# Performance work log

Hardware: AMD Instinct MI355X
Metric: run time of the kernel (lower is better)

The kernel has to match this reference:

```python
import jax, jax.numpy as jnp
from jax import lax
import numpy as np

WIN = 11
SIGMA = 1.5
PAD = WIN // 2
C1 = 0.01 ** 2
C2 = 0.03 ** 2


def _gauss1d():
    x = jnp.arange(WIN, dtype=jnp.float32) - (WIN // 2)
    k = jnp.exp(-(x ** 2) / (2.0 * SIGMA ** 2))
    return k / k.sum()


def _blur3d(x, k1d):
    # Separable 3D gaussian blur (mathematically identical to the outer-product
    # 3D kernel used by the torch module, since kernel3d = k1d (x) k1d (x) k1d).
    # x: [B, 1, D, H, W]
    dn = ('NCDHW', 'OIDHW', 'NCDHW')
    x = lax.conv_general_dilated(x, k1d.reshape(1, 1, WIN, 1, 1), (1, 1, 1),
                                 [(PAD, PAD), (0, 0), (0, 0)], dimension_numbers=dn)
    x = lax.conv_general_dilated(x, k1d.reshape(1, 1, 1, WIN, 1), (1, 1, 1),
                                 [(0, 0), (PAD, PAD), (0, 0)], dimension_numbers=dn)
    x = lax.conv_general_dilated(x, k1d.reshape(1, 1, 1, 1, WIN), (1, 1, 1),
                                 [(0, 0), (0, 0), (PAD, PAD)], dimension_numbers=dn)
    return x


def setup_inputs() -> dict:
    key = jax.random.key(0)
    k1, k2 = jax.random.split(key)
    shape = (2, 1, 192, 192, 192)
    img1 = jax.random.uniform(k1, shape, dtype=jnp.float32)
    img2 = jax.random.uniform(k2, shape, dtype=jnp.float32)
    return {"img1": img1, "img2": img2}


def reference(img1, img2):
    k1d = _gauss1d().astype(img1.dtype)
    mu1 = _blur3d(img1, k1d)
    mu2 = _blur3d(img2, k1d)
    mu1_sq = mu1 * mu1
    mu2_sq = mu2 * mu2
    mu1mu2 = mu1 * mu2
    sigma1 = _blur3d(img1 * img1, k1d) - mu1_sq
    sigma2 = _blur3d(img2 * img2, k1d) - mu2_sq
    sigma12 = _blur3d(img1 * img2, k1d) - mu1mu2
    num = (2.0 * mu1mu2 + C1) * (2.0 * sigma12 + C2)
    den = (mu1_sq + mu2_sq + C1) * (sigma1 + sigma2 + C2)
    ssim_map = num / den
    return ssim_map.mean()  # size_average=True
```

## Files before the change

### kernel.cpp

```cpp
#include <hip/hip_runtime.h>

#define NB 2
#define DD 192
#define HH 192
#define WW 192
#define HWSZ (HH * WW)
#define C1F 0.0001f
#define C2F 0.0009f

#define TH 16
#define TW 32
#define CHUNK 32
#define TSTEPS (CHUNK + 10)
#define NCH (DD / CHUNK)
#define NTH (HH / TH)
#define NTW (WW / TW)
#define NBLK (NB * NCH * NTH * NTW)

#define SROWS (TH + 10)
#define SCOLS 42
#define SP2 44
#define TQ 36
#define NSTG (SROWS * SCOLS)
#define NWT (SROWS * (TW / 4))

#define KWLIST { 0.00102838f, 0.00759876f, 0.03600077f, 0.10936071f, 0.21300556f, \
                 0.26601172f, 0.21300556f, 0.10936071f, 0.03600077f, 0.00759876f, 0.00102838f }

__device__ __forceinline__ float ssim_val(float mu1, float mu2, float A, float Bm) {
  const float mu1sq = mu1 * mu1, mu2sq = mu2 * mu2, mu12 = mu1 * mu2;
  const float num = (2.f * mu12 + C1F) * (0.5f * (A - Bm) - 2.f * mu12 + C2F);
  const float den = (mu1sq + mu2sq + C1F) * (0.5f * (A + Bm) - mu1sq - mu2sq + C2F);
  return num * __builtin_amdgcn_rcpf(den);
}

__global__ __launch_bounds__(256) void ssim_fused(
    const float* __restrict__ x, const float* __restrict__ y,
    float* __restrict__ partials) {
  const float KW[11] = KWLIST;

  int bid = blockIdx.x;
  const int tw = bid % NTW; bid /= NTW;
  const int th = bid % NTH; bid /= NTH;
  const int c  = bid % NCH; bid /= NCH;
  const int b  = bid;
  const int h0 = th * TH, w0 = tw * TW, c0 = c * CHUNK;

  __shared__ __align__(16) float2 s2[SROWS][SP2];
  __shared__ float4 t4[SROWS][TQ];

  const int tid = threadIdx.x;
  const int cl  = tid & 31;
  const int rg  = tid >> 5;
  const int r0  = 2 * rg;
  const int clp2 = (cl & ~3) | (((cl & 3) + (cl >> 2)) & 3);

  int  sIdx[5], sOff[5];
  bool sOk[5];
#pragma unroll
  for (int k = 0; k < 5; ++k) {
    const int q = tid + 256 * k;
    const bool act = (q < NSTG);
    const int row = q / SCOLS, col = q % SCOLS;
    const int gh = h0 - 5 + row, gw = w0 - 5 + col;
    sOk[k]  = act && (unsigned)gh < (unsigned)HH && (unsigned)gw < (unsigned)WW;
    sIdx[k] = row * SP2 + col;
    sOff[k] = gh * WW + gw;
  }
  const bool wAct = (tid < NWT);
  const int  wr = tid >> 3;
  const int  wq = tid & 7;
  const int  tBase = wr * TQ + 4 * wq;
  const int  st0 = tBase + ((0 + wq) & 3);
  const int  st1 = tBase + ((1 + wq) & 3);
  const int  st2 = tBase + ((2 + wq) & 3);
  const int  st3 = tBase + ((3 + wq) & 3);

  {
    const float2 z = make_float2(0.f, 0.f);
    for (int q = tid; q < SROWS * SP2; q += 256) (&s2[0][0])[q] = z;
  }
  __syncthreads();

  const float* xb = x + (size_t)b * DD * HWSZ;
  const float* yb = y + (size_t)b * DD * HWSZ;

  float pend0[4][11], pend1[4][11];
#pragma unroll
  for (int f = 0; f < 4; ++f)
#pragma unroll
    for (int i = 0; i < 11; ++i) { pend0[f][i] = 0.f; pend1[f][i] = 0.f; }

  float px[5], py[5];
#pragma unroll
  for (int k = 0; k < 5; ++k) { px[k] = 0.f; py[k] = 0.f; }

  if (c0 >= 5) {
    const float* xs = xb + (size_t)(c0 - 5) * HWSZ;
    const float* ys = yb + (size_t)(c0 - 5) * HWSZ;
#pragma unroll
    for (int k = 0; k < 5; ++k)
      if (sOk[k]) { px[k] = xs[sOff[k]]; py[k] = ys[sOff[k]]; }
  }

  float lsum = 0.f;
  int p = 0;

  for (int t = 0; t < TSTEPS; ++t) {
    const int d = c0 - 5 + t;
    const bool dv = (d >= 0) && (d < DD);

    if (dv) {
#pragma unroll
      for (int k = 0; k < 5; ++k)
        if (sOk[k]) (&s2[0][0])[sIdx[k]] = make_float2(px[k], py[k]);
    }
    {
      const int dn = d + 1;
      if ((t + 1) < TSTEPS && dn >= 0 && dn < DD) {
        const float* xs = xb + (size_t)dn * HWSZ;
        const float* ys = yb + (size_t)dn * HWSZ;
#pragma unroll
        for (int k = 0; k < 5; ++k)
          if (sOk[k]) { px[k] = xs[sOff[k]]; py[k] = ys[sOff[k]]; }
      }
    }

    float4 B0 = make_float4(0.f, 0.f, 0.f, 0.f);
    float4 B1 = B0;

    if (dv) {
      __syncthreads();
      if (wAct) {
        const float4* srow4 = (const float4*)&s2[wr][0];
        float4 a0 = make_float4(0.f, 0.f, 0.f, 0.f), a1 = a0, a2 = a0, a3 = a0;
#pragma unroll
        for (int u2 = 0; u2 < 7; ++u2) {
          const float4 v2 = srow4[2 * wq + u2];
#pragma unroll
          for (int h = 0; h < 2; ++h) {
            const int   u  = 2 * u2 + h;
            const float xx = h ? v2.z : v2.x;
            const float yy = h ? v2.w : v2.y;
            const float sm = xx + yy, df = xx - yy;
            const float s2q = sm * sm, d2q = df * df;
            if (u <= 10)           { const float k = KW[u];     a0.x += k*xx; a0.y += k*yy; a0.z += k*s2q; a0.w += k*d2q; }
            if (u >= 1 && u <= 11) { const float k = KW[u - 1]; a1.x += k*xx; a1.y += k*yy; a1.z += k*s2q; a1.w += k*d2q; }
            if (u >= 2 && u <= 12) { const float k = KW[u - 2]; a2.x += k*xx; a2.y += k*yy; a2.z += k*s2q; a2.w += k*d2q; }
            if (u >= 3)            { const float k = KW[u - 3]; a3.x += k*xx; a3.y += k*yy; a3.z += k*s2q; a3.w += k*d2q; }
          }
        }
        float4* tb = &t4[0][0];
        tb[st0] = a0; tb[st1] = a1; tb[st2] = a2; tb[st3] = a3;
      }
      __syncthreads();

#pragma unroll
      for (int u = 0; u < 12; ++u) {
        const float4 v = t4[r0 + u][clp2];
        if (u <= 10) { const float k = KW[u];     B0.x += k*v.x; B0.y += k*v.y; B0.z += k*v.z; B0.w += k*v.w; }
        if (u >= 1)  { const float k = KW[u - 1]; B1.x += k*v.x; B1.y += k*v.y; B1.z += k*v.z; B1.w += k*v.w; }
      }
    }

#define RING_CASE(P)                                                        \
    case P: {                                                               \
      if (dv) {                                                             \
        _Pragma("unroll")                                                   \
        for (int kk = 0; kk < 11; ++kk) {                                   \
          const int   sl = (P + 1 + kk) % 11;                               \
          const float wg = KW[kk];                                          \
          pend0[0][sl] += wg * B0.x; pend0[1][sl] += wg * B0.y;             \
          pend0[2][sl] += wg * B0.z; pend0[3][sl] += wg * B0.w;             \
          pend1[0][sl] += wg * B1.x; pend1[1][sl] += wg * B1.y;             \
          pend1[2][sl] += wg * B1.z; pend1[3][sl] += wg * B1.w;             \
        }                                                                   \
      }                                                                     \
      const int sc = (P + 1) % 11;                                          \
      if (t >= 10) {                                                        \
        lsum += ssim_val(pend0[0][sc], pend0[1][sc], pend0[2][sc], pend0[3][sc]); \
        lsum += ssim_val(pend1[0][sc], pend1[1][sc], pend1[2][sc], pend1[3][sc]); \
      }                                                                     \
      pend0[0][sc] = 0.f; pend0[1][sc] = 0.f;                               \
      pend0[2][sc] = 0.f; pend0[3][sc] = 0.f;                               \
      pend1[0][sc] = 0.f; pend1[1][sc] = 0.f;                               \
      pend1[2][sc] = 0.f; pend1[3][sc] = 0.f;                               \
    } break;

    switch (p) {
      RING_CASE(0) RING_CASE(1) RING_CASE(2) RING_CASE(3) RING_CASE(4)
      RING_CASE(5) RING_CASE(6) RING_CASE(7) RING_CASE(8) RING_CASE(9)
      RING_CASE(10)
    }
#undef RING_CASE
    p = (p + 1 == 11) ? 0 : p + 1;
  }

  for (int off = 32; off > 0; off >>= 1) lsum += __shfl_down(lsum, off, 64);
  __shared__ float wsum[4];
  if ((tid & 63) == 0) wsum[tid >> 6] = lsum;
  __syncthreads();
  if (tid == 0) partials[blockIdx.x] = wsum[0] + wsum[1] + wsum[2] + wsum[3];
}

__global__ __launch_bounds__(256) void ssim_reduce(
    const float* __restrict__ partials, float* __restrict__ out) {
  __shared__ double sd[256];
  double a = 0.0;
  for (int i = threadIdx.x; i < NBLK; i += 256) a += (double)partials[i];
  sd[threadIdx.x] = a;
  __syncthreads();
  for (int s = 128; s > 0; s >>= 1) {
    if ((int)threadIdx.x < s) sd[threadIdx.x] += sd[threadIdx.x + s];
    __syncthreads();
  }
  if (threadIdx.x == 0) {
    out[0] = (float)(sd[0] / (double)((size_t)NB * DD * HH * WW));
  }
}

extern "C" void kernel_launch(void* const* d_in, const int* in_sizes, int n_in,
                              void* d_out, int out_size, void* d_ws, size_t ws_size,
                              hipStream_t stream) {
  const float* img1 = (const float*)d_in[0];
  const float* img2 = (const float*)d_in[1];
  float* out = (float*)d_out;
  float* partials = (float*)d_ws;

  ssim_fused<<<NBLK, 256, 0, stream>>>(img1, img2, partials);
  ssim_reduce<<<1, 256, 0, stream>>>(partials, out);
}
```

Measured before the change: 171.9 us.

## Double-buffer staging and W-blur shared buffers to pipeline depth slices

Double-buffers the input staging and W-blur shared-memory tiles so that each depth step stages slice e+2, runs the W-blur on slice e+1 and does the H-blur on slice e, all in one phase. This cuts the two barriers per depth step down to one and lets the prefetch run one slice further ahead. It also adds a per-row 2-float skew to the staging layout, apparently to spread LDS bank accesses. The cost is double the shared-memory footprint, which may reduce occupancy, plus a more complex prologue.

```diff
diff --git a/kernel.cpp b/kernel.cpp
--- a/kernel.cpp
+++ b/kernel.cpp
@@ -46,8 +46,8 @@
   const int b  = bid;
   const int h0 = th * TH, w0 = tw * TW, c0 = c * CHUNK;
 
-  __shared__ __align__(16) float2 s2[SROWS][SP2];
-  __shared__ float4 t4[SROWS][TQ];
+  __shared__ __align__(16) float2 s2[2][SROWS][SP2];
+  __shared__ float4 t4[2][SROWS][TQ];
 
   const int tid = threadIdx.x;
   const int cl  = tid & 31;
@@ -64,7 +64,7 @@
     const int row = q / SCOLS, col = q % SCOLS;
     const int gh = h0 - 5 + row, gw = w0 - 5 + col;
     sOk[k]  = act && (unsigned)gh < (unsigned)HH && (unsigned)gw < (unsigned)WW;
-    sIdx[k] = row * SP2 + col;
+    sIdx[k] = row * SP2 + 2 * (row & 1) + col;
     sOff[k] = gh * WW + gw;
   }
   const bool wAct = (tid < NWT);
@@ -78,86 +78,93 @@
 
   {
     const float2 z = make_float2(0.f, 0.f);
-    for (int q = tid; q < SROWS * SP2; q += 256) (&s2[0][0])[q] = z;
-  }
-  __syncthreads();
+    float2* sb = &s2[0][0][0];
+    for (int q = tid; q < 2 * SROWS * SP2; q += 256) sb[q] = z;
+  }
 
   const float* xb = x + (size_t)b * DD * HWSZ;
   const float* yb = y + (size_t)b * DD * HWSZ;
 
-  float pend0[4][11], pend1[4][11];
-#pragma unroll
-  for (int f = 0; f < 4; ++f)
-#pragma unroll
-    for (int i = 0; i < 11; ++i) { pend0[f][i] = 0.f; pend1[f][i] = 0.f; }
-
   float px[5], py[5];
 #pragma unroll
   for (int k = 0; k < 5; ++k) { px[k] = 0.f; py[k] = 0.f; }
 
-  if (c0 >= 5) {
-    const float* xs = xb + (size_t)(c0 - 5) * HWSZ;
-    const float* ys = yb + (size_t)(c0 - 5) * HWSZ;
+  auto do_prefetch = [&](int g) {
+    const float* xs = xb + (size_t)g * HWSZ;
+    const float* ys = yb + (size_t)g * HWSZ;
 #pragma unroll
     for (int k = 0; k < 5; ++k)
       if (sOk[k]) { px[k] = xs[sOff[k]]; py[k] = ys[sOff[k]]; }
-  }
+  };
+  auto do_stage = [&](float2* s2buf) {
+#pragma unroll
+    for (int k = 0; k < 5; ++k)
+      if (sOk[k]) s2buf[sIdx[k]] = make_float2(px[k], py[k]);
+  };
+  auto do_wblur = [&](const float2* s2buf, float4* t4buf) {
+    if (wAct) {
+      const float4* srow4 = (const float4*)(s2buf + wr * SP2 + 2 * (wr & 1));
+      float4 a0 = make_float4(0.f, 0.f, 0.f, 0.f), a1 = a0, a2 = a0, a3 = a0;
+#pragma unroll
+      for (int u2 = 0; u2 < 7; ++u2) {
+        const float4 v2 = srow4[2 * wq + u2];
+#pragma unroll
+        for (int h = 0; h < 2; ++h) {
+          const int   u  = 2 * u2 + h;
+          const float xx = h ? v2.z : v2.x;
+          const float yy = h ? v2.w : v2.y;
+          const float sm = xx + yy, df = xx - yy;
+          const float sq = sm * sm, dq = df * df;
+          if (u <= 10)           { const float k = KW[u];     a0.x += k*xx; a0.y += k*yy; a0.z += k*sq; a0.w += k*dq; }
+          if (u >= 1 && u <= 11) { const float k = KW[u - 1]; a1.x += k*xx; a1.y += k*yy; a1.z += k*sq; a1.w += k*dq; }
+          if (u >= 2 && u <= 12) { const float k = KW[u - 2]; a2.x += k*xx; a2.y += k*yy; a2.z += k*sq; a2.w += k*dq; }
+          if (u >= 3)            { const float k = KW[u - 3]; a3.x += k*xx; a3.y += k*yy; a3.z += k*sq; a3.w += k*dq; }
+        }
+      }
+      t4buf[st0] = a0; t4buf[st1] = a1; t4buf[st2] = a2; t4buf[st3] = a3;
+    }
+  };
+
+  float pend0[4][11], pend1[4][11];
+#pragma unroll
+  for (int f = 0; f < 4; ++f)
+#pragma unroll
+    for (int i = 0; i < 11; ++i) { pend0[f][i] = 0.f; pend1[f][i] = 0.f; }
 
   float lsum = 0.f;
+
+  __syncthreads();
+  if (c0 - 5 >= 0) do_prefetch(c0 - 5);
+  if (c0 - 5 >= 0) do_stage(&s2[1][0][0]);
+  if (c0 - 4 >= 0) do_prefetch(c0 - 4);
+  __syncthreads();
+  if (c0 - 5 >= 0) do_wblur(&s2[1][0][0], &t4[0][0][0]);
+  if (c0 - 4 >= 0) do_stage(&s2[0][0][0]);
+  if (c0 - 3 >= 0) do_prefetch(c0 - 3);
+  __syncthreads();
+
   int p = 0;
-
-  for (int t = 0; t < TSTEPS; ++t) {
-    const int d = c0 - 5 + t;
-    const bool dv = (d >= 0) && (d < DD);
-
-    if (dv) {
-#pragma unroll
-      for (int k = 0; k < 5; ++k)
-        if (sOk[k]) (&s2[0][0])[sIdx[k]] = make_float2(px[k], py[k]);
-    }
-    {
-      const int dn = d + 1;
-      if ((t + 1) < TSTEPS && dn >= 0 && dn < DD) {
-        const float* xs = xb + (size_t)dn * HWSZ;
-        const float* ys = yb + (size_t)dn * HWSZ;
-#pragma unroll
-        for (int k = 0; k < 5; ++k)
-          if (sOk[k]) { px[k] = xs[sOff[k]]; py[k] = ys[sOff[k]]; }
-      }
-    }
+  for (int j = 0; j < TSTEPS; ++j) {
+    const int cb = j & 1, nb = cb ^ 1;
+    const int e = c0 - 5 + j;
+    const int d = e + 1;
+    const int g = e + 2;
+    const bool eOK = (e >= 0) && (e < DD);
+    const bool dOK = (j <= 40) && (d >= 0) && (d < DD);
+    const bool gOK = (j <= 39) && (g >= 0) && (g < DD);
+    const bool g2OK = (j <= 38) && (g + 1 >= 0) && (g + 1 < DD);
+
+    if (gOK) do_stage(&s2[nb][0][0]);
+    if (g2OK) do_prefetch(g + 1);
+    if (dOK) do_wblur(&s2[cb][0][0], &t4[nb][0][0]);
 
     float4 B0 = make_float4(0.f, 0.f, 0.f, 0.f);
     float4 B1 = B0;
-
-    if (dv) {
-      __syncthreads();
-      if (wAct) {
-        const float4* srow4 = (const float4*)&s2[wr][0];
-        float4 a0 = make_float4(0.f, 0.f, 0.f, 0.f), a1 = a0, a2 = a0, a3 = a0;
-#pragma unroll
-        for (int u2 = 0; u2 < 7; ++u2) {
-          const float4 v2 = srow4[2 * wq + u2];
-#pragma unroll
-          for (int h = 0; h < 2; ++h) {
-            const int   u  = 2 * u2 + h;
-            const float xx = h ? v2.z : v2.x;
-            const float yy = h ? v2.w : v2.y;
-            const float sm = xx + yy, df = xx - yy;
-            const float s2q = sm * sm, d2q = df * df;
-            if (u <= 10)           { const float k = KW[u];     a0.x += k*xx; a0.y += k*yy; a0.z += k*s2q; a0.w += k*d2q; }
-            if (u >= 1 && u <= 11) { const float k = KW[u - 1]; a1.x += k*xx; a1.y += k*yy; a1.z += k*s2q; a1.w += k*d2q; }
-            if (u >= 2 && u <= 12) { const float k = KW[u - 2]; a2.x += k*xx; a2.y += k*yy; a2.z += k*s2q; a2.w += k*d2q; }
-            if (u >= 3)            { const float k = KW[u - 3]; a3.x += k*xx; a3.y += k*yy; a3.z += k*s2q; a3.w += k*d2q; }
-          }
-        }
-        float4* tb = &t4[0][0];
-        tb[st0] = a0; tb[st1] = a1; tb[st2] = a2; tb[st3] = a3;
-      }
-      __syncthreads();
-
+    if (eOK) {
+      const float4* tb = &t4[cb][0][0];
 #pragma unroll
       for (int u = 0; u < 12; ++u) {
-        const float4 v = t4[r0 + u][clp2];
+        const float4 v = tb[(r0 + u) * TQ + clp2];
         if (u <= 10) { const float k = KW[u];     B0.x += k*v.x; B0.y += k*v.y; B0.z += k*v.z; B0.w += k*v.w; }
         if (u >= 1)  { const float k = KW[u - 1]; B1.x += k*v.x; B1.y += k*v.y; B1.z += k*v.z; B1.w += k*v.w; }
       }
@@ -165,7 +172,7 @@
 
 #define RING_CASE(P)                                                        \
     case P: {                                                               \
-      if (dv) {                                                             \
+      if (eOK) {                                                            \
         _Pragma("unroll")                                                   \
         for (int kk = 0; kk < 11; ++kk) {                                   \
           const int   sl = (P + 1 + kk) % 11;                               \
@@ -177,7 +184,7 @@
         }                                                                   \
       }                                                                     \
       const int sc = (P + 1) % 11;                                          \
-      if (t >= 10) {                                                        \
+      if (j >= 10) {                                                        \
         lsum += ssim_val(pend0[0][sc], pend0[1][sc], pend0[2][sc], pend0[3][sc]); \
         lsum += ssim_val(pend1[0][sc], pend1[1][sc], pend1[2][sc], pend1[3][sc]); \
       }                                                                     \
@@ -194,6 +201,8 @@
     }
 #undef RING_CASE
     p = (p + 1 == 11) ? 0 : p + 1;
+
+    __syncthreads();
   }
 
   for (int off = 32; off > 0; off >>= 1) lsum += __shfl_down(lsum, off, 64);
```

Result: faster. 167.5 us (-2.6%).
